# Kernel tuning notes

Measured on AMD Instinct MI355X. Metric: run time of the kernel, lower is better.

Reference implementation:

```python
import jax, jax.numpy as jnp
import numpy as np

B, T, KQ, KT, NDOF = 1024, 1024, 15, 20, 7


def huber(x, delta=1.0):
    ax = jnp.abs(x)
    return jnp.where(ax < delta, 0.5 * x * x, delta * (ax - 0.5 * delta))


def setup_inputs() -> dict:
    key = jax.random.key(0)
    ks = jax.random.split(key, 12)
    q_cps = jax.random.normal(ks[0], (B, KQ, NDOF), dtype=jnp.float32)
    # time-spline control points must be positive so dtau_dt > 0
    t_cps = jax.random.uniform(ks[1], (B, KT, 1), dtype=jnp.float32) + 0.5
    # B-spline basis matrices for q(tau): [1, T, KQ]
    N = jax.random.normal(ks[2], (1, T, KQ), dtype=jnp.float32)
    dN = jax.random.normal(ks[3], (1, T, KQ), dtype=jnp.float32)
    ddN = jax.random.normal(ks[4], (1, T, KQ), dtype=jnp.float32)
    dddN = jax.random.normal(ks[5], (1, T, KQ), dtype=jnp.float32)
    # time-spline basis: Nt nonnegative so dtau_dt stays positive
    Nt = jax.random.uniform(ks[6], (1, T, KT), dtype=jnp.float32)
    dNt = jax.random.normal(ks[7], (1, T, KT), dtype=jnp.float32)
    ddNt = jax.random.normal(ks[8], (1, T, KT), dtype=jnp.float32)
    q_dot_limits = jnp.array([1.4835, 1.4835, 1.7453, 1.3090, 2.2689, 2.3562, 2.3562], dtype=jnp.float32)
    q_ddot_limits = 10.0 * q_dot_limits
    q_dddot_limits = 100.0 * q_dot_limits
    torque_limits = jnp.array([320.0, 320.0, 176.0, 176.0, 110.0, 40.0, 40.0], dtype=jnp.float32)
    return {"q_cps": q_cps, "t_cps": t_cps, "N": N, "dN": dN, "ddN": ddN,
            "dddN": dddN, "Nt": Nt, "dNt": dNt, "ddNt": ddNt,
            "q_dot_limits": q_dot_limits, "q_ddot_limits": q_ddot_limits,
            "q_dddot_limits": q_dddot_limits, "torque_limits": torque_limits}


def reference(q_cps, t_cps, N, dN, ddN, dddN, Nt, dNt, ddNt,
              q_dot_limits, q_ddot_limits, q_dddot_limits, torque_limits):
    # spline evaluations: [B, T, NDOF] and [B, T, 1]
    q = jnp.einsum('ijk,lkm->ljm', N, q_cps)
    q_dot_tau = jnp.einsum('ijk,lkm->ljm', dN, q_cps)
    q_ddot_tau = jnp.einsum('ijk,lkm->ljm', ddN, q_cps)
    q_dddot_tau = jnp.einsum('ijk,lkm->ljm', dddN, q_cps)
    dtau_dt = jnp.einsum('ijk,lkm->ljm', Nt, t_cps)
    ddtau_dtt = jnp.einsum('ijk,lkm->ljm', dNt, t_cps)
    dddtau_dttt = jnp.einsum('ijk,lkm->ljm', ddNt, t_cps)

    dt = 1.0 / dtau_dt[..., 0] / dtau_dt.shape[1]  # [B, T]
    t_cumsum = jnp.cumsum(dt, axis=-1)
    t = jnp.sum(dt, axis=-1)

    dtau_dt2 = dtau_dt ** 2
    q_dot = q_dot_tau * dtau_dt
    q_ddot = q_ddot_tau * dtau_dt2 + ddtau_dtt * q_dot_tau * dtau_dt
    q_dddot = (q_dddot_tau * dtau_dt ** 3
               + 3.0 * q_ddot_tau * ddtau_dtt * dtau_dt2
               + q_dot_tau * dtau_dt2 * dddtau_dttt
               + q_dot_tau * ddtau_dtt ** 2 * dtau_dt)

    # original rnea() returns zeros as the forward torque value
    torque = jnp.zeros_like(q)

    dt_e = dt[..., None]  # [B, T, 1]
    torque_loss = jnp.sum(huber(jax.nn.relu(jnp.abs(torque) - torque_limits)) * dt_e, axis=1)
    q_dot_loss = jnp.sum(huber(jax.nn.relu(jnp.abs(q_dot) - q_dot_limits)) * dt_e, axis=1)
    q_ddot_loss = jnp.sum(huber(jax.nn.relu(jnp.abs(q_ddot) - q_ddot_limits)) * dt_e, axis=1)
    q_dddot_loss = jnp.sum(huber(jax.nn.relu(jnp.abs(q_dddot) - q_dddot_limits)) * dt_e, axis=1)

    model_losses = jnp.concatenate([q_dot_loss, q_ddot_loss, q_dddot_loss], axis=-1)
    model_loss = jnp.sum(model_losses)
    return (model_loss, q_dot_loss, q_ddot_loss, q_dddot_loss, torque_loss,
            q, q_dot, q_ddot, q_dddot, torque, t, t_cumsum, dt)
```

## Files before the change

kernel.cpp:

```cpp
#include <hip/hip_runtime.h>

#define BB 1024
#define TT 1024
#define KQ 15
#define KT 20
#define KTP 21
#define NDOF 7
#define TTILE 64
#define NTTILE (TT/TTILE)
#define BW 4
#define NBGRP (BB/BW)

#define OFF_MODEL 0
#define OFF_QDL   1
#define OFF_QDDL  (1 + BB*NDOF)
#define OFF_QDDDL (1 + 2*BB*NDOF)
#define OFF_TQL   (1 + 3*BB*NDOF)
#define OFF_Q     (1 + 4*BB*NDOF)
#define OFF_QD    (OFF_Q    + (size_t)BB*TT*NDOF)
#define OFF_QDD   (OFF_QD   + (size_t)BB*TT*NDOF)
#define OFF_QDDD  (OFF_QDD  + (size_t)BB*TT*NDOF)
#define OFF_TQ    (OFF_QDDD + (size_t)BB*TT*NDOF)
#define OFF_T     (OFF_TQ   + (size_t)BB*TT*NDOF)
#define OFF_TCUM  (OFF_T    + (size_t)BB)
#define OFF_DT    (OFF_TCUM + (size_t)BB*TT)

#define WS_LOSS   0
#define WS_BSUM   ((size_t)BB * NTTILE * 21)

__device__ __forceinline__ float hub(float v, float lim) {
    float x = fabsf(v) - lim;
    x = fmaxf(x, 0.0f);
    return (x < 1.0f) ? 0.5f * x * x : (x - 0.5f);
}

__device__ __forceinline__ void st4(float* p, float x0, float x1, float x2, float x3) {
    float v[4] = {x0, x1, x2, x3};
    __builtin_memcpy(p, v, 16);
}

__global__ __launch_bounds__(256, 2) void feas_main(
    const float* __restrict__ q_cps, const float* __restrict__ t_cps,
    const float* __restrict__ Nb,  const float* __restrict__ dNb,
    const float* __restrict__ ddNb, const float* __restrict__ dddNb,
    const float* __restrict__ Ntb, const float* __restrict__ dNtb,
    const float* __restrict__ ddNtb,
    const float* __restrict__ qd_lim, const float* __restrict__ qdd_lim,
    const float* __restrict__ qddd_lim,
    float* __restrict__ out, float* __restrict__ lws)
{
    const int ttile = blockIdx.x;
    const int bgrp  = blockIdx.y;
    const int tid   = threadIdx.x;
    const int lane  = tid & 63;
    const int w     = tid >> 6;
    const int bw = __builtin_amdgcn_readfirstlane(bgrp * BW + w);

    __shared__ __align__(16) float smem[3840 + 3 * TTILE * KTP];
    float* qb = smem;
    float* tb = smem + 3840;

    {
        const size_t gq = (size_t)ttile * (TTILE * KQ);
        if (tid < 240) {
            const float4 v0 = *(const float4*)(Nb    + gq + tid * 4);
            const float4 v1 = *(const float4*)(dNb   + gq + tid * 4);
            const float4 v2 = *(const float4*)(ddNb  + gq + tid * 4);
            const float4 v3 = *(const float4*)(dddNb + gq + tid * 4);
            *(float4*)(qb + 0 * TTILE * KQ + tid * 4) = v0;
            *(float4*)(qb + 1 * TTILE * KQ + tid * 4) = v1;
            *(float4*)(qb + 2 * TTILE * KQ + tid * 4) = v2;
            *(float4*)(qb + 3 * TTILE * KQ + tid * 4) = v3;
        }
        const size_t gt = (size_t)ttile * (TTILE * KT);
        #pragma unroll
        for (int j = 0; j < 5; ++j) {
            const unsigned g = (unsigned)(j * 256 + tid);
            const unsigned t = g / 20u;
            const unsigned k = g - t * 20u;
            const unsigned l = t * KTP + k;
            tb[0 * TTILE * KTP + l] = Ntb [gt + g];
            tb[1 * TTILE * KTP + l] = dNtb[gt + g];
            tb[2 * TTILE * KTP + l] = ddNtb[gt + g];
        }
    }
    __syncthreads();

    const float* cps = q_cps + (size_t)bw * KQ * NDOF;
    const float* tcp = t_cps + (size_t)bw * KT;

    float dtau = 0.f, ddtau = 0.f, dddtau = 0.f;
    {
        const float* p = tb + lane * KTP;
        #pragma unroll
        for (int k = 0; k < KT; ++k) {
            const float tc = tcp[k];
            dtau   = fmaf(p[k],                   tc, dtau);
            ddtau  = fmaf(p[1 * TTILE * KTP + k], tc, ddtau);
            dddtau = fmaf(p[2 * TTILE * KTP + k], tc, dddtau);
        }
    }

    float aq[NDOF], a1[NDOF], a2[NDOF], a3[NDOF];
    #pragma unroll
    for (int d = 0; d < NDOF; ++d) { aq[d] = 0.f; a1[d] = 0.f; a2[d] = 0.f; a3[d] = 0.f; }
    {
        const float* p = qb + lane * KQ;
        #pragma unroll
        for (int k = 0; k < KQ; ++k) {
            const float n0 = p[k];
            const float n1 = p[1 * TTILE * KQ + k];
            const float n2 = p[2 * TTILE * KQ + k];
            const float n3 = p[3 * TTILE * KQ + k];
            #pragma unroll
            for (int d = 0; d < NDOF; ++d) {
                const float cc = cps[k * NDOF + d];
                aq[d] = fmaf(n0, cc, aq[d]);
                a1[d] = fmaf(n1, cc, a1[d]);
                a2[d] = fmaf(n2, cc, a2[d]);
                a3[d] = fmaf(n3, cc, a3[d]);
            }
        }
    }

    const float dtau2 = dtau * dtau;
    const float dtau3 = dtau2 * dtau;
    const float dtv   = 1.0f / (dtau * (float)TT);

    float qd[NDOF], qdd[NDOF], qddd[NDOF];
    #pragma unroll
    for (int d = 0; d < NDOF; ++d) {
        qd[d]   = a1[d] * dtau;
        qdd[d]  = a2[d] * dtau2 + ddtau * a1[d] * dtau;
        qddd[d] = a3[d] * dtau3 + 3.0f * a2[d] * ddtau * dtau2
                + a1[d] * dtau2 * dddtau + a1[d] * ddtau * ddtau * dtau;
    }

    out[OFF_DT + (size_t)bw * TT + ttile * TTILE + lane] = dtv;

    {
        float ls[21];
        #pragma unroll
        for (int d = 0; d < NDOF; ++d) {
            ls[d]          = hub(qd[d],   qd_lim[d])   * dtv;
            ls[NDOF + d]   = hub(qdd[d],  qdd_lim[d])  * dtv;
            ls[2*NDOF + d] = hub(qddd[d], qddd_lim[d]) * dtv;
        }
        #pragma unroll
        for (int j = 0; j < 21; ++j) {
            float v = ls[j];
            #pragma unroll
            for (int off = 32; off > 0; off >>= 1) v += __shfl_down(v, off);
            ls[j] = v;
        }
        if (lane == 0) {
            float* wp = lws + WS_LOSS + ((size_t)bw * NTTILE + ttile) * 21;
            #pragma unroll
            for (int j = 0; j < 21; ++j) wp[j] = ls[j];
        }
    }

    __syncthreads();
    {
        float* r = smem + (size_t)(w * 4) * (TTILE * NDOF) + lane * NDOF;
        #pragma unroll
        for (int d = 0; d < NDOF; ++d) {
            r[0 * TTILE * NDOF + d] = aq[d];
            r[1 * TTILE * NDOF + d] = qd[d];
            r[2 * TTILE * NDOF + d] = qdd[d];
            r[3 * TTILE * NDOF + d] = qddd[d];
        }
    }
    __syncthreads();
    {
        const size_t gb = (size_t)bw * (TT * NDOF) + (size_t)ttile * (TTILE * NDOF);
        const float* rb = smem + (size_t)(w * 4) * (TTILE * NDOF);
        #pragma unroll
        for (int a = 0; a < 4; ++a) {
            const size_t off = (a == 0) ? (size_t)OFF_Q : (a == 1) ? (size_t)OFF_QD
                             : (a == 2) ? (size_t)OFF_QDD : (size_t)OFF_QDDD;
            const float* s = rb + a * (TTILE * NDOF);
            const float4 x0 = *(const float4*)(s + lane * 4);
            st4(out + off + gb + lane * 4, x0.x, x0.y, x0.z, x0.w);
            if (lane < 48) {
                const float4 x1 = *(const float4*)(s + 256 + lane * 4);
                st4(out + off + gb + 256 + lane * 4, x1.x, x1.y, x1.z, x1.w);
            }
        }
        st4(out + OFF_TQ + gb + lane * 4, 0.f, 0.f, 0.f, 0.f);
        if (lane < 48) st4(out + OFF_TQ + gb + 256 + lane * 4, 0.f, 0.f, 0.f, 0.f);
    }
}

__global__ __launch_bounds__(256) void feas_scan(
    float* __restrict__ out, const float* __restrict__ lws, float* __restrict__ bsum)
{
    __shared__ float sb[TT];
    __shared__ float seg[256];
    __shared__ float lsum[21];
    const int b   = blockIdx.x;
    const int tid = threadIdx.x;

    const int s4 = 4 * tid;
    const size_t dtb = OFF_DT + (size_t)b * TT;
    const float d0 = out[dtb + s4 + 0];
    const float d1 = out[dtb + s4 + 1];
    const float d2 = out[dtb + s4 + 2];
    const float d3 = out[dtb + s4 + 3];
    const float c0 = d0;
    const float c1 = c0 + d1;
    const float c2 = c1 + d2;
    const float c3 = c2 + d3;

    seg[tid] = c3;
    __syncthreads();
    #pragma unroll
    for (int off = 1; off < 256; off <<= 1) {
        float v = 0.0f;
        if (tid >= off) v = seg[tid - off];
        __syncthreads();
        if (tid >= off) seg[tid] += v;
        __syncthreads();
    }
    const float excl  = (tid > 0) ? seg[tid - 1] : 0.0f;
    const float total = seg[255];

    sb[s4 + 0] = c0 + excl;
    sb[s4 + 1] = c1 + excl;
    sb[s4 + 2] = c2 + excl;
    sb[s4 + 3] = c3 + excl;

    if (tid < 21) {
        const float* wp = lws + WS_LOSS + (size_t)b * NTTILE * 21 + tid;
        float s = 0.f;
        #pragma unroll
        for (int tt = 0; tt < NTTILE; ++tt) s += wp[tt * 21];
        const int which = tid / NDOF, d = tid - which * NDOF;
        const size_t o = (which == 0) ? (size_t)OFF_QDL
                       : (which == 1) ? (size_t)OFF_QDDL : (size_t)OFF_QDDDL;
        out[o + (size_t)b * NDOF + d] = s;
        lsum[tid] = s;
    }
    if (tid < NDOF) out[OFF_TQL + (size_t)b * NDOF + tid] = 0.0f;
    __syncthreads();

    const size_t tb = OFF_TCUM + (size_t)b * TT;
    #pragma unroll
    for (int j = 0; j < 4; ++j) {
        const int f = j * 256 + tid;
        out[tb + f] = sb[f];
    }
    if (tid == 0) {
        out[OFF_T + b] = total;
        float p = 0.f;
        #pragma unroll
        for (int j = 0; j < 21; ++j) p += lsum[j];
        bsum[b] = p;
    }
}

__global__ __launch_bounds__(256) void feas_final(
    const float* __restrict__ bsum, float* __restrict__ out)
{
    __shared__ float wsums[4];
    const int tid  = threadIdx.x;
    const int lane = tid & 63;
    const int w    = tid >> 6;
    float v = 0.f;
    #pragma unroll
    for (int j = 0; j < 4; ++j) v += bsum[j * 256 + tid];
    #pragma unroll
    for (int off = 32; off > 0; off >>= 1) v += __shfl_down(v, off);
    if (lane == 0) wsums[w] = v;
    __syncthreads();
    if (tid == 0) out[OFF_MODEL] = wsums[0] + wsums[1] + wsums[2] + wsums[3];
}

extern "C" void kernel_launch(void* const* d_in, const int* in_sizes, int n_in,
                              void* d_out, int out_size, void* d_ws, size_t ws_size,
                              hipStream_t stream) {
    const float* q_cps    = (const float*)d_in[0];
    const float* t_cps    = (const float*)d_in[1];
    const float* Nb       = (const float*)d_in[2];
    const float* dNb      = (const float*)d_in[3];
    const float* ddNb     = (const float*)d_in[4];
    const float* dddNb    = (const float*)d_in[5];
    const float* Ntb      = (const float*)d_in[6];
    const float* dNtb     = (const float*)d_in[7];
    const float* ddNtb    = (const float*)d_in[8];
    const float* qd_lim   = (const float*)d_in[9];
    const float* qdd_lim  = (const float*)d_in[10];
    const float* qddd_lim = (const float*)d_in[11];
    float* out = (float*)d_out;
    float* lws = (float*)d_ws;

    feas_main<<<dim3(NTTILE, NBGRP), dim3(256), 0, stream>>>(
        q_cps, t_cps, Nb, dNb, ddNb, dddNb, Ntb, dNtb, ddNtb,
        qd_lim, qdd_lim, qddd_lim, out, lws);
    feas_scan<<<dim3(BB), dim3(256), 0, stream>>>(out, lws, lws + WS_BSUM);
    feas_final<<<dim3(1), dim3(256), 0, stream>>>(lws + WS_BSUM, out);
}
```

Baseline: 222.2 us.

## Fuse spline evaluation and cumsum scan into one per-batch kernel

Replaces the tiled main kernel plus separate scan kernel with one kernel where each block handles one batch row across all timesteps. The cumsum and loss reductions happen in-block with wave shuffles, so dt is no longer re-read from global memory and one launch and the workspace round trip go away. In exchange, basis matrices are read straight from global memory per thread with no shared-memory staging. The outputs are now written with uncoalesced 7-float stride stores (16/8/4-byte pieces) rather than coalesced float4 stores staged through LDS, which may hurt write bandwidth on a store-bound kernel.

```diff
diff --git a/kernel.cpp b/kernel.cpp
--- a/kernel.cpp
+++ b/kernel.cpp
@@ -4,12 +4,7 @@
 #define TT 1024
 #define KQ 15
 #define KT 20
-#define KTP 21
 #define NDOF 7
-#define TTILE 64
-#define NTTILE (TT/TTILE)
-#define BW 4
-#define NBGRP (BB/BW)
 
 #define OFF_MODEL 0
 #define OFF_QDL   1
@@ -25,9 +20,6 @@
 #define OFF_TCUM  (OFF_T    + (size_t)BB)
 #define OFF_DT    (OFF_TCUM + (size_t)BB*TT)
 
-#define WS_LOSS   0
-#define WS_BSUM   ((size_t)BB * NTTILE * 21)
-
 __device__ __forceinline__ float hub(float v, float lim) {
     float x = fabsf(v) - lim;
     x = fmaxf(x, 0.0f);
@@ -39,7 +31,15 @@
     __builtin_memcpy(p, v, 16);
 }
 
-__global__ __launch_bounds__(256, 2) void feas_main(
+__device__ __forceinline__ void st7(float* p, const float* a) {
+    float v4[4] = {a[0], a[1], a[2], a[3]};
+    __builtin_memcpy(p, v4, 16);
+    float v2[2] = {a[4], a[5]};
+    __builtin_memcpy(p + 4, v2, 8);
+    p[6] = a[6];
+}
+
+__global__ __launch_bounds__(256, 4) void feas_fused(
     const float* __restrict__ q_cps, const float* __restrict__ t_cps,
     const float* __restrict__ Nb,  const float* __restrict__ dNb,
     const float* __restrict__ ddNb, const float* __restrict__ dddNb,
@@ -47,71 +47,54 @@
     const float* __restrict__ ddNtb,
     const float* __restrict__ qd_lim, const float* __restrict__ qdd_lim,
     const float* __restrict__ qddd_lim,
-    float* __restrict__ out, float* __restrict__ lws)
+    float* __restrict__ out, float* __restrict__ bsum)
 {
-    const int ttile = blockIdx.x;
-    const int bgrp  = blockIdx.y;
-    const int tid   = threadIdx.x;
-    const int lane  = tid & 63;
-    const int w     = tid >> 6;
-    const int bw = __builtin_amdgcn_readfirstlane(bgrp * BW + w);
-
-    __shared__ __align__(16) float smem[3840 + 3 * TTILE * KTP];
-    float* qb = smem;
-    float* tb = smem + 3840;
-
-    {
-        const size_t gq = (size_t)ttile * (TTILE * KQ);
-        if (tid < 240) {
-            const float4 v0 = *(const float4*)(Nb    + gq + tid * 4);
-            const float4 v1 = *(const float4*)(dNb   + gq + tid * 4);
-            const float4 v2 = *(const float4*)(ddNb  + gq + tid * 4);
-            const float4 v3 = *(const float4*)(dddNb + gq + tid * 4);
-            *(float4*)(qb + 0 * TTILE * KQ + tid * 4) = v0;
-            *(float4*)(qb + 1 * TTILE * KQ + tid * 4) = v1;
-            *(float4*)(qb + 2 * TTILE * KQ + tid * 4) = v2;
-            *(float4*)(qb + 3 * TTILE * KQ + tid * 4) = v3;
-        }
-        const size_t gt = (size_t)ttile * (TTILE * KT);
-        #pragma unroll
-        for (int j = 0; j < 5; ++j) {
-            const unsigned g = (unsigned)(j * 256 + tid);
-            const unsigned t = g / 20u;
-            const unsigned k = g - t * 20u;
-            const unsigned l = t * KTP + k;
-            tb[0 * TTILE * KTP + l] = Ntb [gt + g];
-            tb[1 * TTILE * KTP + l] = dNtb[gt + g];
-            tb[2 * TTILE * KTP + l] = ddNtb[gt + g];
-        }
-    }
-    __syncthreads();
-
-    const float* cps = q_cps + (size_t)bw * KQ * NDOF;
-    const float* tcp = t_cps + (size_t)bw * KT;
-
-    float dtau = 0.f, ddtau = 0.f, dddtau = 0.f;
-    {
-        const float* p = tb + lane * KTP;
+    const int b    = blockIdx.x;
+    const int tid  = threadIdx.x;
+    const int lane = tid & 63;
+    const int w    = tid >> 6;
+
+    __shared__ __align__(16) float sdt[TT];
+    __shared__ float wsum[4];
+    __shared__ float lossw[4][21];
+
+    const float* cps = q_cps + (size_t)b * (KQ * NDOF);
+    const float* tcp = t_cps + (size_t)b * KT;
+
+    float tcr[KT];
+    #pragma unroll
+    for (int k = 0; k < KT; ++k) tcr[k] = tcp[k];
+
+    float ls[21];
+    #pragma unroll
+    for (int j = 0; j < 21; ++j) ls[j] = 0.f;
+
+    #pragma unroll 1
+    for (int r = 0; r < TT / 256; ++r) {
+        const int t = r * 256 + tid;
+
+        const float* pt0 = Ntb   + (size_t)t * KT;
+        const float* pt1 = dNtb  + (size_t)t * KT;
+        const float* pt2 = ddNtb + (size_t)t * KT;
+        float dtau = 0.f, ddtau = 0.f, dddtau = 0.f;
         #pragma unroll
         for (int k = 0; k < KT; ++k) {
-            const float tc = tcp[k];
-            dtau   = fmaf(p[k],                   tc, dtau);
-            ddtau  = fmaf(p[1 * TTILE * KTP + k], tc, ddtau);
-            dddtau = fmaf(p[2 * TTILE * KTP + k], tc, dddtau);
-        }
-    }
-
-    float aq[NDOF], a1[NDOF], a2[NDOF], a3[NDOF];
-    #pragma unroll
-    for (int d = 0; d < NDOF; ++d) { aq[d] = 0.f; a1[d] = 0.f; a2[d] = 0.f; a3[d] = 0.f; }
-    {
-        const float* p = qb + lane * KQ;
+            const float tc = tcr[k];
+            dtau   = fmaf(pt0[k], tc, dtau);
+            ddtau  = fmaf(pt1[k], tc, ddtau);
+            dddtau = fmaf(pt2[k], tc, dddtau);
+        }
+
+        const float* p0 = Nb    + (size_t)t * KQ;
+        const float* p1 = dNb   + (size_t)t * KQ;
+        const float* p2 = ddNb  + (size_t)t * KQ;
+        const float* p3 = dddNb + (size_t)t * KQ;
+        float aq[NDOF], a1[NDOF], a2[NDOF], a3[NDOF];
+        #pragma unroll
+        for (int d = 0; d < NDOF; ++d) { aq[d] = 0.f; a1[d] = 0.f; a2[d] = 0.f; a3[d] = 0.f; }
         #pragma unroll
         for (int k = 0; k < KQ; ++k) {
-            const float n0 = p[k];
-            const float n1 = p[1 * TTILE * KQ + k];
-            const float n2 = p[2 * TTILE * KQ + k];
-            const float n3 = p[3 * TTILE * KQ + k];
+            const float n0 = p0[k], n1 = p1[k], n2 = p2[k], n3 = p3[k];
             #pragma unroll
             for (int d = 0; d < NDOF; ++d) {
                 const float cc = cps[k * NDOF + d];
@@ -121,140 +104,96 @@
                 a3[d] = fmaf(n3, cc, a3[d]);
             }
         }
-    }
-
-    const float dtau2 = dtau * dtau;
-    const float dtau3 = dtau2 * dtau;
-    const float dtv   = 1.0f / (dtau * (float)TT);
-
-    float qd[NDOF], qdd[NDOF], qddd[NDOF];
-    #pragma unroll
-    for (int d = 0; d < NDOF; ++d) {
-        qd[d]   = a1[d] * dtau;
-        qdd[d]  = a2[d] * dtau2 + ddtau * a1[d] * dtau;
-        qddd[d] = a3[d] * dtau3 + 3.0f * a2[d] * ddtau * dtau2
-                + a1[d] * dtau2 * dddtau + a1[d] * ddtau * ddtau * dtau;
-    }
-
-    out[OFF_DT + (size_t)bw * TT + ttile * TTILE + lane] = dtv;
-
-    {
-        float ls[21];
+
+        const float dtau2 = dtau * dtau;
+        const float dtau3 = dtau2 * dtau;
+        const float dtv   = 1.0f / (dtau * (float)TT);
+
+        float qd[NDOF], qdd[NDOF], qddd[NDOF];
         #pragma unroll
         for (int d = 0; d < NDOF; ++d) {
-            ls[d]          = hub(qd[d],   qd_lim[d])   * dtv;
-            ls[NDOF + d]   = hub(qdd[d],  qdd_lim[d])  * dtv;
-            ls[2*NDOF + d] = hub(qddd[d], qddd_lim[d]) * dtv;
-        }
-        #pragma unroll
-        for (int j = 0; j < 21; ++j) {
-            float v = ls[j];
-            #pragma unroll
-            for (int off = 32; off > 0; off >>= 1) v += __shfl_down(v, off);
-            ls[j] = v;
-        }
-        if (lane == 0) {
-            float* wp = lws + WS_LOSS + ((size_t)bw * NTTILE + ttile) * 21;
-            #pragma unroll
-            for (int j = 0; j < 21; ++j) wp[j] = ls[j];
-        }
+            qd[d]   = a1[d] * dtau;
+            qdd[d]  = a2[d] * dtau2 + ddtau * a1[d] * dtau;
+            qddd[d] = a3[d] * dtau3 + 3.0f * a2[d] * ddtau * dtau2
+                    + a1[d] * dtau2 * dddtau + a1[d] * ddtau * ddtau * dtau;
+        }
+
+        #pragma unroll
+        for (int d = 0; d < NDOF; ++d) {
+            ls[d]          += hub(qd[d],   qd_lim[d])   * dtv;
+            ls[NDOF + d]   += hub(qdd[d],  qdd_lim[d])  * dtv;
+            ls[2*NDOF + d] += hub(qddd[d], qddd_lim[d]) * dtv;
+        }
+
+        const size_t gb = (size_t)b * (TT * NDOF) + (size_t)t * NDOF;
+        st7(out + OFF_Q    + gb, aq);
+        st7(out + OFF_QD   + gb, qd);
+        st7(out + OFF_QDD  + gb, qdd);
+        st7(out + OFF_QDDD + gb, qddd);
+        {
+            float* z = out + OFF_TQ + gb;
+            st4(z, 0.f, 0.f, 0.f, 0.f);
+            float v2[2] = {0.f, 0.f};
+            __builtin_memcpy(z + 4, v2, 8);
+            z[6] = 0.f;
+        }
+        out[OFF_DT + (size_t)b * TT + t] = dtv;
+        sdt[t] = dtv;
     }
 
     __syncthreads();
-    {
-        float* r = smem + (size_t)(w * 4) * (TTILE * NDOF) + lane * NDOF;
-        #pragma unroll
-        for (int d = 0; d < NDOF; ++d) {
-            r[0 * TTILE * NDOF + d] = aq[d];
-            r[1 * TTILE * NDOF + d] = qd[d];
-            r[2 * TTILE * NDOF + d] = qdd[d];
-            r[3 * TTILE * NDOF + d] = qddd[d];
-        }
-    }
+
+    const int s4 = 4 * tid;
+    const float4 dvv = *(const float4*)(sdt + s4);
+    const float c0 = dvv.x;
+    const float c1 = c0 + dvv.y;
+    const float c2 = c1 + dvv.z;
+    const float c3 = c2 + dvv.w;
+    float s = c3;
+    #pragma unroll
+    for (int off = 1; off < 64; off <<= 1) {
+        const float u = __shfl_up(s, off);
+        if (lane >= off) s += u;
+    }
+    if (lane == 63) wsum[w] = s;
+
+    #pragma unroll
+    for (int j = 0; j < 21; ++j) {
+        float v = ls[j];
+        #pragma unroll
+        for (int off = 32; off > 0; off >>= 1) v += __shfl_down(v, off);
+        ls[j] = v;
+    }
+    if (lane == 0) {
+        #pragma unroll
+        for (int j = 0; j < 21; ++j) lossw[w][j] = ls[j];
+    }
+
     __syncthreads();
-    {
-        const size_t gb = (size_t)bw * (TT * NDOF) + (size_t)ttile * (TTILE * NDOF);
-        const float* rb = smem + (size_t)(w * 4) * (TTILE * NDOF);
-        #pragma unroll
-        for (int a = 0; a < 4; ++a) {
-            const size_t off = (a == 0) ? (size_t)OFF_Q : (a == 1) ? (size_t)OFF_QD
-                             : (a == 2) ? (size_t)OFF_QDD : (size_t)OFF_QDDD;
-            const float* s = rb + a * (TTILE * NDOF);
-            const float4 x0 = *(const float4*)(s + lane * 4);
-            st4(out + off + gb + lane * 4, x0.x, x0.y, x0.z, x0.w);
-            if (lane < 48) {
-                const float4 x1 = *(const float4*)(s + 256 + lane * 4);
-                st4(out + off + gb + 256 + lane * 4, x1.x, x1.y, x1.z, x1.w);
-            }
-        }
-        st4(out + OFF_TQ + gb + lane * 4, 0.f, 0.f, 0.f, 0.f);
-        if (lane < 48) st4(out + OFF_TQ + gb + 256 + lane * 4, 0.f, 0.f, 0.f, 0.f);
-    }
-}
-
-__global__ __launch_bounds__(256) void feas_scan(
-    float* __restrict__ out, const float* __restrict__ lws, float* __restrict__ bsum)
-{
-    __shared__ float sb[TT];
-    __shared__ float seg[256];
-    __shared__ float lsum[21];
-    const int b   = blockIdx.x;
-    const int tid = threadIdx.x;
-
-    const int s4 = 4 * tid;
-    const size_t dtb = OFF_DT + (size_t)b * TT;
-    const float d0 = out[dtb + s4 + 0];
-    const float d1 = out[dtb + s4 + 1];
-    const float d2 = out[dtb + s4 + 2];
-    const float d3 = out[dtb + s4 + 3];
-    const float c0 = d0;
-    const float c1 = c0 + d1;
-    const float c2 = c1 + d2;
-    const float c3 = c2 + d3;
-
-    seg[tid] = c3;
-    __syncthreads();
-    #pragma unroll
-    for (int off = 1; off < 256; off <<= 1) {
-        float v = 0.0f;
-        if (tid >= off) v = seg[tid - off];
-        __syncthreads();
-        if (tid >= off) seg[tid] += v;
-        __syncthreads();
-    }
-    const float excl  = (tid > 0) ? seg[tid - 1] : 0.0f;
-    const float total = seg[255];
-
-    sb[s4 + 0] = c0 + excl;
-    sb[s4 + 1] = c1 + excl;
-    sb[s4 + 2] = c2 + excl;
-    sb[s4 + 3] = c3 + excl;
+
+    float woff = 0.f;
+    #pragma unroll
+    for (int i = 0; i < 4; ++i) if (i < w) woff += wsum[i];
+    const float excl = woff + (s - c3);
+    st4(out + OFF_TCUM + (size_t)b * TT + s4,
+        c0 + excl, c1 + excl, c2 + excl, c3 + excl);
 
     if (tid < 21) {
-        const float* wp = lws + WS_LOSS + (size_t)b * NTTILE * 21 + tid;
-        float s = 0.f;
-        #pragma unroll
-        for (int tt = 0; tt < NTTILE; ++tt) s += wp[tt * 21];
+        const float acc = lossw[0][tid] + lossw[1][tid] + lossw[2][tid] + lossw[3][tid];
         const int which = tid / NDOF, d = tid - which * NDOF;
         const size_t o = (which == 0) ? (size_t)OFF_QDL
                        : (which == 1) ? (size_t)OFF_QDDL : (size_t)OFF_QDDDL;
-        out[o + (size_t)b * NDOF + d] = s;
-        lsum[tid] = s;
+        out[o + (size_t)b * NDOF + d] = acc;
     }
     if (tid < NDOF) out[OFF_TQL + (size_t)b * NDOF + tid] = 0.0f;
-    __syncthreads();
-
-    const size_t tb = OFF_TCUM + (size_t)b * TT;
-    #pragma unroll
-    for (int j = 0; j < 4; ++j) {
-        const int f = j * 256 + tid;
-        out[tb + f] = sb[f];
-    }
     if (tid == 0) {
-        out[OFF_T + b] = total;
+        out[OFF_T + b] = wsum[0] + wsum[1] + wsum[2] + wsum[3];
         float p = 0.f;
         #pragma unroll
-        for (int j = 0; j < 21; ++j) p += lsum[j];
+        for (int i = 0; i < 4; ++i) {
+            #pragma unroll
+            for (int j = 0; j < 21; ++j) p += lossw[i][j];
+        }
         bsum[b] = p;
     }
 }
@@ -291,12 +230,11 @@
     const float* qd_lim   = (const float*)d_in[9];
     const float* qdd_lim  = (const float*)d_in[10];
     const float* qddd_lim = (const float*)d_in[11];
-    float* out = (float*)d_out;
-    float* lws = (float*)d_ws;
-
-    feas_main<<<dim3(NTTILE, NBGRP), dim3(256), 0, stream>>>(
+    float* out  = (float*)d_out;
+    float* bsum = (float*)d_ws;
+
+    feas_fused<<<dim3(BB), dim3(256), 0, stream>>>(
         q_cps, t_cps, Nb, dNb, ddNb, dddNb, Ntb, dNtb, ddNtb,
-        qd_lim, qdd_lim, qddd_lim, out, lws);
-    feas_scan<<<dim3(BB), dim3(256), 0, stream>>>(out, lws, lws + WS_BSUM);
-    feas_final<<<dim3(1), dim3(256), 0, stream>>>(lws + WS_BSUM, out);
-}
+        qd_lim, qdd_lim, qddd_lim, out, bsum);
+    feas_final<<<dim3(1), dim3(256), 0, stream>>>(bsum, out);
+}
```

New measurement: 236.3 us. +6.3%, slower.
